# Optimization experiments

Hardware: AMD Instinct MI355X
Metric: run time of the kernel (lower is better)

Reference implementation:

```python
import jax, jax.numpy as jnp
import numpy as np

B = 1
FRAMES = 16
P = 64            # patch_dim = image_size // patch_size = 256 // 4
C = 512           # query_dim == hidden_dim
T, HW, WW = 2, 8, 8   # window_size
NH = 8            # num_heads
HD = C // NH      # head_dim = 64
N = FRAMES * P * P


def setup_inputs() -> dict:
    key = jax.random.key(0)
    ks = jax.random.split(key, 5)
    x = jax.random.normal(ks[0], (B, N, C), dtype=jnp.float32)
    Wq = jax.random.normal(ks[1], (C, C), dtype=jnp.float32) * 0.02
    Wk = jax.random.normal(ks[2], (C, C), dtype=jnp.float32) * 0.02
    Wv = jax.random.normal(ks[3], (C, C), dtype=jnp.float32) * 0.02
    Wo = jax.random.normal(ks[4], (C, C), dtype=jnp.float32) * 0.02
    bo = jnp.zeros((C,), dtype=jnp.float32)
    return {"x": x, "Wq": Wq, "Wk": Wk, "Wv": Wv, "Wo": Wo, "bo": bo}


def reference(x, Wq, Wk, Wv, Wo, bo):
    nT, nH, nW = FRAMES // T, P // HW, P // WW
    L = T * HW * WW            # tokens per window = 128
    NWIN = nT * nH * nW        # 512 windows

    # window partition: [B,N,C] -> [B,nWin,L,C]
    xw = x.reshape(B, nT, T, nH, HW, nW, WW, C)
    xw = xw.transpose(0, 1, 3, 5, 2, 4, 6, 7).reshape(B, NWIN, L, C)

    # QKV projections (torch Linear: y = x @ W.T), split heads
    q = (xw @ Wq.T).reshape(B, NWIN, L, NH, HD)
    k = (xw @ Wk.T).reshape(B, NWIN, L, NH, HD)
    v = (xw @ Wv.T).reshape(B, NWIN, L, NH, HD)

    scale = 1.0 / jnp.sqrt(jnp.float32(HD))
    attn = jnp.einsum('bwqhd,bwkhd->bwhqk', q, k) * scale
    attn = jax.nn.softmax(attn, axis=-1)
    out = jnp.einsum('bwhqk,bwkhd->bwqhd', attn, v).reshape(B, NWIN, L, C)

    out = out @ Wo.T + bo      # output projection (dropout is identity at p=0/eval)

    # window merge: inverse of partition
    y = out.reshape(B, nT, nH, nW, T, HW, WW, C)
    y = y.transpose(0, 1, 4, 2, 5, 3, 6, 7).reshape(B, N, C)
    return y
```

## Files before the change

### kernel.cpp

```cpp
#include <hip/hip_runtime.h>


typedef __bf16 bf16x8 __attribute__((ext_vector_type(8)));
typedef float  f32x4  __attribute__((ext_vector_type(4)));

__device__ __forceinline__ unsigned short f2bf(float f) {
    unsigned int u = __float_as_uint(f);
    u += 0x7FFFu + ((u >> 16) & 1u);
    return (unsigned short)(u >> 16);
}
__device__ __forceinline__ unsigned int pack2(float lo, float hi) {
    return (unsigned int)f2bf(lo) | ((unsigned int)f2bf(hi) << 16);
}
__device__ __forceinline__ void glds16(const void* g, void* l) {
    __builtin_amdgcn_global_load_lds(
        (const __attribute__((address_space(1))) unsigned int*)g,
        (__attribute__((address_space(3))) unsigned int*)l, 16, 0, 0);
}

__global__ __launch_bounds__(256) void gather_cvt(const float* __restrict__ x,
                                                  unsigned short* __restrict__ xbf) {
    int tid = blockIdx.x * 256 + threadIdx.x;
    int r = tid >> 6;
    int c = (tid & 63) << 3;
    int w = r >> 7, l = r & 127;
    int wt = w >> 6, wy = (w >> 3) & 7, wx = w & 7;
    int lt = l >> 6, ly = (l >> 3) & 7, lx = l & 7;
    size_t n = (size_t)(wt * 2 + lt) * 4096 + (size_t)(wy * 8 + ly) * 64 + (wx * 8 + lx);
    const float4* s = (const float4*)(x + n * 512 + c);
    float4 a = s[0], b = s[1];
    uint4 o;
    o.x = pack2(a.x, a.y); o.y = pack2(a.z, a.w);
    o.z = pack2(b.x, b.y); o.w = pack2(b.z, b.w);
    *(uint4*)(xbf + (size_t)r * 512 + c) = o;
}

__global__ __launch_bounds__(256) void cvt_w4(const float* __restrict__ Wq,
                                              const float* __restrict__ Wk,
                                              const float* __restrict__ Wv,
                                              const float* __restrict__ Wo,
                                              unsigned short* __restrict__ d) {
    int b = blockIdx.x >> 7;
    int tid = (blockIdx.x & 127) * 256 + threadIdx.x;
    const float* s = (b == 0) ? Wq : (b == 1) ? Wk : (b == 2) ? Wv : Wo;
    const float4* sp = (const float4*)s + (size_t)tid * 2;
    float4 a = sp[0], bb = sp[1];
    uint4 o;
    o.x = pack2(a.x, a.y); o.y = pack2(a.z, a.w);
    o.z = pack2(bb.x, bb.y); o.w = pack2(bb.z, bb.w);
    ((uint4*)(d + (size_t)b * 262144))[tid] = o;
}


#define STAGE_A(tt, kh) do {                                                   \
    const unsigned short* g_ = Ap + (size_t)(tt) * 64 + (kh) * 32 + gOff;      \
    unsigned short* l_ = smem + ((((tt) & 1) * 2 + (kh)) * 8192);              \
    glds16(g_, l_ + j * 8);                                                    \
    glds16(g_ + 65536, l_ + 4096 + j * 8);                                     \
  } while (0)

#define STAGE_B(tt, kh) do {                                                   \
    const unsigned short* g_ = Bp + (size_t)(tt) * 64 + (kh) * 32 + gOff;      \
    unsigned short* l_ = smem + 32768 + ((((tt) & 1) * 2 + (kh)) * 8192);      \
    glds16(g_, l_ + j * 8);                                                    \
    glds16(g_ + 65536, l_ + 4096 + j * 8);                                     \
  } while (0)

#define PH_READA(d, ks, mh)                                                    \
    _Pragma("unroll") for (int i_ = 0; i_ < 4; ++i_)                           \
      af[i_] = *(const bf16x8*)(smem + ((d) * 2 + (ks)) * 8192 +               \
                                (arow + (mh) * 64 + i_ * 16) * 32 + ech);

#define PH_READB(d, ks)                                                        \
    _Pragma("unroll") for (int n_ = 0; n_ < 4; ++n_)                           \
      bfr[n_] = *(const bf16x8*)(smem + 32768 + ((d) * 2 + (ks)) * 8192 +      \
                                 (brow + n_ * 16) * 32 + ech);

#define PH_MFMA(mh)                                                            \
    __builtin_amdgcn_s_barrier();                                              \
    asm volatile("s_waitcnt lgkmcnt(0)" ::: "memory");                         \
    __builtin_amdgcn_sched_barrier(0);                                         \
    __builtin_amdgcn_s_setprio(1);                                             \
    _Pragma("unroll") for (int n_ = 0; n_ < 4; ++n_)                           \
      _Pragma("unroll") for (int i_ = 0; i_ < 4; ++i_)                         \
        acc[(mh) * 4 + i_][n_] = __builtin_amdgcn_mfma_f32_16x16x32_bf16(      \
            af[i_], bfr[n_], acc[(mh) * 4 + i_][n_], 0, 0, 0);                 \
    __builtin_amdgcn_s_setprio(0);                                             \
    __builtin_amdgcn_s_barrier();

__global__ __launch_bounds__(512, 2) void qkv_gemm8(const unsigned short* __restrict__ xbf,
                                                    const unsigned short* __restrict__ wb,
                                                    unsigned short* __restrict__ Qb,
                                                    unsigned short* __restrict__ Kb,
                                                    unsigned short* __restrict__ Vb) {
    extern __shared__ unsigned short smem[];
    int id = blockIdx.x;
    int xcd = id & 7, rest = id >> 3;
    int rowblk = xcd * 32 + rest / 6;
    int colblk = rest % 6;

    const unsigned short* Ap = xbf + (size_t)rowblk * 131072;
    const unsigned short* Bp = wb + (size_t)colblk * 131072;

    int j = threadIdx.x;
    int lane = j & 63, wv = j >> 6;
    int wm = wv >> 2, wn = wv & 3;
    int quad = lane >> 4, lc = lane & 15;

    int r0 = j >> 2;
    int dcol = (((j & 3) ^ ((j >> 3) & 3)) << 3);
    const size_t gOff = (size_t)r0 * 512 + dcol;

    int arow = wm * 128 + lc;
    int brow = wn * 64 + lc;
    int ech = (quad ^ ((lc >> 1) & 3)) << 3;

    f32x4 acc[8][4] = {};
    bf16x8 af[4], bfr[4];

    STAGE_A(0, 0); STAGE_B(0, 0); STAGE_A(0, 1); STAGE_B(0, 1);
    STAGE_A(1, 0); STAGE_B(1, 0);
    asm volatile("s_waitcnt vmcnt(4)" ::: "memory");
    __builtin_amdgcn_s_barrier();

    #pragma unroll 2
    for (int t = 0; t < 8; ++t) {
        const int d = t & 1;
        PH_READA(d, 0, 0); PH_READB(d, 0);
        if (t < 7) STAGE_A(t + 1, 1);
        PH_MFMA(0);
        PH_READA(d, 0, 1);
        if (t < 7) {
            STAGE_B(t + 1, 1);
            asm volatile("s_waitcnt vmcnt(4)" ::: "memory");
        }
        PH_MFMA(1);
        PH_READA(d, 1, 0); PH_READB(d, 1);
        if (t < 6) STAGE_A(t + 2, 0);
        PH_MFMA(0);
        PH_READA(d, 1, 1);
        if (t < 6) {
            STAGE_B(t + 2, 0);
            asm volatile("s_waitcnt vmcnt(4)" ::: "memory");
        } else if (t == 6) {
            asm volatile("s_waitcnt vmcnt(0)" ::: "memory");
        }
        PH_MFMA(1);
    }

    unsigned short* sc = smem + wv * 8192;
    int cb = colblk * 256 + wn * 64;
    int pj = cb >> 9;
    int h = (cb >> 6) & 7;
    int w2 = rowblk * 2 + wm;
    size_t ob = ((size_t)w2 * 8 + h) * 8192;

    if (pj == 2) {
        #pragma unroll
        for (int mi = 0; mi < 8; ++mi)
            #pragma unroll
            for (int n = 0; n < 4; ++n)
                #pragma unroll
                for (int rg = 0; rg < 4; ++rg) {
                    int l = mi * 16 + quad * 4 + rg;
                    int d2 = n * 16 + lc;
                    sc[d2 * 128 + (((l >> 3) ^ (d2 & 7)) << 3) + (l & 7)] =
                        f2bf(acc[mi][n][rg]);
                }
        asm volatile("s_waitcnt lgkmcnt(0)" ::: "memory");
        #pragma unroll
        for (int i = 0; i < 16; ++i) {
            int ci = i * 64 + lane;
            int d2 = ci >> 4, k = ci & 15;
            uint4 val = *(const uint4*)(sc + d2 * 128 + ((k ^ (d2 & 7)) << 3));
            *(uint4*)(Vb + ob + (size_t)ci * 8) = val;
        }
    } else {
        unsigned short* outp = pj ? Kb : Qb;
        float s = pj ? 1.0f : 0.125f;
        #pragma unroll
        for (int mi = 0; mi < 8; ++mi)
            #pragma unroll
            for (int n = 0; n < 4; ++n)
                #pragma unroll
                for (int rg = 0; rg < 4; ++rg) {
                    int l = mi * 16 + quad * 4 + rg;
                    int d2 = n * 16 + lc;
                    sc[l * 64 + (((d2 >> 3) ^ (l & 7)) << 3) + (d2 & 7)] =
                        f2bf(acc[mi][n][rg] * s);
                }
        asm volatile("s_waitcnt lgkmcnt(0)" ::: "memory");
        #pragma unroll
        for (int i = 0; i < 16; ++i) {
            int ci = i * 64 + lane;
            int l = ci >> 3, k = ci & 7;
            uint4 val = *(const uint4*)(sc + l * 64 + ((k ^ (l & 7)) << 3));
            *(uint4*)(outp + ob + (size_t)ci * 8) = val;
        }
    }
}

__global__ __launch_bounds__(256) void attn(const unsigned short* __restrict__ Qb,
                                            const unsigned short* __restrict__ Kb,
                                            const unsigned short* __restrict__ Vb,
                                            unsigned short* __restrict__ O) {
    int h = blockIdx.x, w = blockIdx.y;
    size_t base = ((size_t)w * 8 + h) * 8192;
    const unsigned short* q = Qb + base;
    const unsigned short* k = Kb + base;
    const unsigned short* v = Vb + base;

    __shared__ unsigned short smem[24576];
    unsigned short* sV = smem;
    unsigned short* sQ = smem + 8192;
    unsigned short* sK = smem + 16384;
    unsigned short* sP = smem + 8192;

    int t = threadIdx.x, lane = t & 63, wv = t >> 6;
    int quad = lane >> 4, lc = lane & 15;
    int sw = lc & 7;

    #pragma unroll
    for (int i = 0; i < 4; i++) {
        int s = t + i * 256;
        int r = s >> 3;
        int cq = ((s & 7) ^ (r & 7)) * 8;
        glds16(q + (size_t)r * 64 + cq, sQ + s * 8);
        glds16(k + (size_t)r * 64 + cq, sK + s * 8);
        int rv = s >> 4;
        int cv = (((s & 15) ^ (rv & 7))) * 8;
        glds16(v + (size_t)rv * 128 + cv, sV + s * 8);
    }
    __syncthreads();

    f32x4 acc[2][8] = {};
    #pragma unroll
    for (int ks = 0; ks < 2; ks++) {
        int ch = ((quad + ks * 4) ^ sw) * 8;
        bf16x8 af[2];
        #pragma unroll
        for (int mi = 0; mi < 2; mi++)
            af[mi] = *(const bf16x8*)(&sQ[(wv * 32 + mi * 16 + lc) * 64 + ch]);
        #pragma unroll
        for (int ni = 0; ni < 8; ni++) {
            bf16x8 bfr = *(const bf16x8*)(&sK[(ni * 16 + lc) * 64 + ch]);
            #pragma unroll
            for (int mi = 0; mi < 2; mi++)
                acc[mi][ni] = __builtin_amdgcn_mfma_f32_16x16x32_bf16(af[mi], bfr, acc[mi][ni], 0, 0, 0);
        }
    }

    #pragma unroll
    for (int mi = 0; mi < 2; mi++)
        #pragma unroll
        for (int rg = 0; rg < 4; rg++) {
            float m = -1e30f;
            #pragma unroll
            for (int ni = 0; ni < 8; ni++) m = fmaxf(m, acc[mi][ni][rg]);
            #pragma unroll
            for (int off = 1; off < 16; off <<= 1) m = fmaxf(m, __shfl_xor(m, off, 64));
            float s = 0.f;
            #pragma unroll
            for (int ni = 0; ni < 8; ni++) {
                float e = __expf(acc[mi][ni][rg] - m);
                acc[mi][ni][rg] = e;
                s += e;
            }
            #pragma unroll
            for (int off = 1; off < 16; off <<= 1) s += __shfl_xor(s, off, 64);
            float inv = 1.0f / s;
            #pragma unroll
            for (int ni = 0; ni < 8; ni++) acc[mi][ni][rg] *= inv;
        }

    __syncthreads();
    #pragma unroll
    for (int mi = 0; mi < 2; mi++)
        #pragma unroll
        for (int ni = 0; ni < 8; ni++)
            #pragma unroll
            for (int rg = 0; rg < 4; rg++) {
                int r = wv * 32 + mi * 16 + quad * 4 + rg;
                int c = ni * 16 + lc;
                sP[r * 128 + (((c >> 3) ^ (r & 7)) << 3) + (c & 7)] = f2bf(acc[mi][ni][rg]);
            }
    __syncthreads();

    f32x4 oc[2][4] = {};
    #pragma unroll
    for (int ks = 0; ks < 4; ks++) {
        int ch = ((quad + ks * 4) ^ sw) * 8;
        bf16x8 af[2];
        #pragma unroll
        for (int mi = 0; mi < 2; mi++)
            af[mi] = *(const bf16x8*)(&sP[(wv * 32 + mi * 16 + lc) * 128 + ch]);
        #pragma unroll
        for (int ni = 0; ni < 4; ni++) {
            bf16x8 bfr = *(const bf16x8*)(&sV[(ni * 16 + lc) * 128 + ch]);
            #pragma unroll
            for (int mi = 0; mi < 2; mi++)
                oc[mi][ni] = __builtin_amdgcn_mfma_f32_16x16x32_bf16(af[mi], bfr, oc[mi][ni], 0, 0, 0);
        }
    }

    #pragma unroll
    for (int mi = 0; mi < 2; mi++)
        #pragma unroll
        for (int ni = 0; ni < 4; ni++)
            #pragma unroll
            for (int rg = 0; rg < 4; rg++) {
                int l = wv * 32 + mi * 16 + quad * 4 + rg;
                int d = ni * 16 + lc;
                O[((size_t)w * 128 + l) * 512 + h * 64 + d] = f2bf(oc[mi][ni][rg]);
            }
}

__global__ __launch_bounds__(256) void oproj_gemm(const unsigned short* __restrict__ A,
                                                  const unsigned short* __restrict__ Bw,
                                                  const float* __restrict__ bo,
                                                  float* __restrict__ out) {
    int id = blockIdx.x;
    int xcd = id & 7, rest = id >> 3;
    int rb = xcd * 64 + (rest >> 2);
    int nb = rest & 3;
    const unsigned short* Ab = A + (size_t)rb * 128 * 512;
    const unsigned short* Bb = Bw + (size_t)nb * 128 * 512;
    __shared__ unsigned short sA[128 * 64];
    __shared__ unsigned short sB[128 * 64];
    f32x4 acc[4][4] = {};
    int t = threadIdx.x, lane = t & 63, wv = t >> 6;
    int wm = wv & 1, wn = wv >> 1, quad = lane >> 4, lc = lane & 15;
    int sw = lc & 7;

    int sr = t >> 3;
    int gco = ((t & 7) ^ (sr & 7)) * 8;

    for (int k0 = 0; k0 < 512; k0 += 64) {
        __syncthreads();
        #pragma unroll
        for (int i = 0; i < 4; i++) {
            int r = sr + i * 32;
            glds16(Ab + (size_t)r * 512 + k0 + gco, sA + (t + i * 256) * 8);
            glds16(Bb + (size_t)r * 512 + k0 + gco, sB + (t + i * 256) * 8);
        }
        __syncthreads();
        #pragma unroll
        for (int ks = 0; ks < 2; ks++) {
            int ch = ((quad + ks * 4) ^ sw) * 8;
            bf16x8 af[4], bfr[4];
            #pragma unroll
            for (int i = 0; i < 4; i++) {
                af[i]  = *(const bf16x8*)(&sA[(wm * 64 + i * 16 + lc) * 64 + ch]);
                bfr[i] = *(const bf16x8*)(&sB[(wn * 64 + i * 16 + lc) * 64 + ch]);
            }
            #pragma unroll
            for (int mi = 0; mi < 4; mi++)
                #pragma unroll
                for (int ni = 0; ni < 4; ni++)
                    acc[mi][ni] = __builtin_amdgcn_mfma_f32_16x16x32_bf16(af[mi], bfr[ni], acc[mi][ni], 0, 0, 0);
        }
    }

    float bias[4];
    #pragma unroll
    for (int ni = 0; ni < 4; ni++)
        bias[ni] = bo[nb * 128 + wn * 64 + ni * 16 + lc];

    #pragma unroll
    for (int mi = 0; mi < 4; mi++)
        #pragma unroll
        for (int rg = 0; rg < 4; rg++) {
            int r = rb * 128 + wm * 64 + mi * 16 + quad * 4 + rg;
            int w = r >> 7, l = r & 127;
            int wt = w >> 6, wy = (w >> 3) & 7, wx = w & 7;
            int lt = l >> 6, ly = (l >> 3) & 7, lx = l & 7;
            size_t n = (size_t)(wt * 2 + lt) * 4096 + (size_t)(wy * 8 + ly) * 64 + (wx * 8 + lx);
            #pragma unroll
            for (int ni = 0; ni < 4; ni++) {
                int col = nb * 128 + wn * 64 + ni * 16 + lc;
                out[n * 512 + col] = acc[mi][ni][rg] + bias[ni];
            }
        }
}

extern "C" void kernel_launch(void* const* d_in, const int* in_sizes, int n_in,
                              void* d_out, int out_size, void* d_ws, size_t ws_size,
                              hipStream_t stream) {
    const float* x  = (const float*)d_in[0];
    const float* Wq = (const float*)d_in[1];
    const float* Wk = (const float*)d_in[2];
    const float* Wv = (const float*)d_in[3];
    const float* Wo = (const float*)d_in[4];
    const float* bo = (const float*)d_in[5];
    float* out = (float*)d_out;

    char* ws = (char*)d_ws;
    unsigned short* xbf = (unsigned short*)(ws);
    unsigned short* Qb  = (unsigned short*)(ws + 67108864);
    unsigned short* Kb  = (unsigned short*)(ws + 134217728);
    unsigned short* Vb  = (unsigned short*)(ws + 201326592);
    unsigned short* Wqb = (unsigned short*)(ws + 268435456);

    static bool attrset = false;
    if (!attrset) {
        (void)hipFuncSetAttribute(reinterpret_cast<const void*>(qkv_gemm8),
                                  hipFuncAttributeMaxDynamicSharedMemorySize, 131072);
        attrset = true;
    }

    gather_cvt<<<16384, 256, 0, stream>>>(x, xbf);
    cvt_w4<<<512, 256, 0, stream>>>(Wq, Wk, Wv, Wo, Wqb);

    qkv_gemm8<<<1536, 512, 131072, stream>>>(xbf, Wqb, Qb, Kb, Vb);
    attn<<<dim3(8, 512), 256, 0, stream>>>(Qb, Kb, Vb, xbf);
    oproj_gemm<<<2048, 256, 0, stream>>>(xbf, Wqb + 786432, bo, out);
}
```

Before: 474.0 us.

## Reuse pipelined 256x256 GEMM for output projection and shrink attention LDS

The output projection GEMM is rewritten to use the same 512-thread, 256x256-tile, double-buffered main loop as the QKV GEMM, shared through a macro. The 128x128 tile kernel it replaces synchronized on every K step. The attention kernel now loads Q fragments straight from global into registers and reuses the K buffer for P, processing P in two halves. This cuts LDS from 48KB to 32KB to raise occupancy. The cost is more register pressure, and the oproj grid drops to 512 large blocks, which may under-fill the device.

```diff
diff --git a/kernel.cpp b/kernel.cpp
--- a/kernel.cpp
+++ b/kernel.cpp
@@ -88,6 +88,36 @@
     __builtin_amdgcn_s_setprio(0);                                             \
     __builtin_amdgcn_s_barrier();
 
+#define GEMM8_MAIN_LOOP                                                        \
+    STAGE_A(0, 0); STAGE_B(0, 0); STAGE_A(0, 1); STAGE_B(0, 1);                \
+    STAGE_A(1, 0); STAGE_B(1, 0);                                              \
+    asm volatile("s_waitcnt vmcnt(4)" ::: "memory");                           \
+    __builtin_amdgcn_s_barrier();                                              \
+    _Pragma("unroll 2")                                                        \
+    for (int t = 0; t < 8; ++t) {                                              \
+        const int d = t & 1;                                                   \
+        PH_READA(d, 0, 0); PH_READB(d, 0);                                     \
+        if (t < 7) STAGE_A(t + 1, 1);                                          \
+        PH_MFMA(0);                                                            \
+        PH_READA(d, 0, 1);                                                     \
+        if (t < 7) {                                                           \
+            STAGE_B(t + 1, 1);                                                 \
+            asm volatile("s_waitcnt vmcnt(4)" ::: "memory");                   \
+        }                                                                      \
+        PH_MFMA(1);                                                            \
+        PH_READA(d, 1, 0); PH_READB(d, 1);                                     \
+        if (t < 6) STAGE_A(t + 2, 0);                                          \
+        PH_MFMA(0);                                                            \
+        PH_READA(d, 1, 1);                                                     \
+        if (t < 6) {                                                           \
+            STAGE_B(t + 2, 0);                                                 \
+            asm volatile("s_waitcnt vmcnt(4)" ::: "memory");                   \
+        } else if (t == 6) {                                                   \
+            asm volatile("s_waitcnt vmcnt(0)" ::: "memory");                   \
+        }                                                                      \
+        PH_MFMA(1);                                                            \
+    }
+
 __global__ __launch_bounds__(512, 2) void qkv_gemm8(const unsigned short* __restrict__ xbf,
                                                     const unsigned short* __restrict__ wb,
                                                     unsigned short* __restrict__ Qb,
@@ -118,35 +148,7 @@
     f32x4 acc[8][4] = {};
     bf16x8 af[4], bfr[4];
 
-    STAGE_A(0, 0); STAGE_B(0, 0); STAGE_A(0, 1); STAGE_B(0, 1);
-    STAGE_A(1, 0); STAGE_B(1, 0);
-    asm volatile("s_waitcnt vmcnt(4)" ::: "memory");
-    __builtin_amdgcn_s_barrier();
-
-    #pragma unroll 2
-    for (int t = 0; t < 8; ++t) {
-        const int d = t & 1;
-        PH_READA(d, 0, 0); PH_READB(d, 0);
-        if (t < 7) STAGE_A(t + 1, 1);
-        PH_MFMA(0);
-        PH_READA(d, 0, 1);
-        if (t < 7) {
-            STAGE_B(t + 1, 1);
-            asm volatile("s_waitcnt vmcnt(4)" ::: "memory");
-        }
-        PH_MFMA(1);
-        PH_READA(d, 1, 0); PH_READB(d, 1);
-        if (t < 6) STAGE_A(t + 2, 0);
-        PH_MFMA(0);
-        PH_READA(d, 1, 1);
-        if (t < 6) {
-            STAGE_B(t + 2, 0);
-            asm volatile("s_waitcnt vmcnt(4)" ::: "memory");
-        } else if (t == 6) {
-            asm volatile("s_waitcnt vmcnt(0)" ::: "memory");
-        }
-        PH_MFMA(1);
-    }
+    GEMM8_MAIN_LOOP
 
     unsigned short* sc = smem + wv * 8192;
     int cb = colblk * 256 + wn * 64;
@@ -210,11 +212,9 @@
     const unsigned short* k = Kb + base;
     const unsigned short* v = Vb + base;
 
-    __shared__ unsigned short smem[24576];
+    __shared__ unsigned short smem[16384];
     unsigned short* sV = smem;
-    unsigned short* sQ = smem + 8192;
-    unsigned short* sK = smem + 16384;
-    unsigned short* sP = smem + 8192;
+    unsigned short* sKP = smem + 8192;
 
     int t = threadIdx.x, lane = t & 63, wv = t >> 6;
     int quad = lane >> 4, lc = lane & 15;
@@ -225,28 +225,31 @@
         int s = t + i * 256;
         int r = s >> 3;
         int cq = ((s & 7) ^ (r & 7)) * 8;
-        glds16(q + (size_t)r * 64 + cq, sQ + s * 8);
-        glds16(k + (size_t)r * 64 + cq, sK + s * 8);
+        glds16(k + (size_t)r * 64 + cq, sKP + s * 8);
         int rv = s >> 4;
         int cv = (((s & 15) ^ (rv & 7))) * 8;
         glds16(v + (size_t)rv * 128 + cv, sV + s * 8);
     }
+
+    bf16x8 aq[2][2];
+    #pragma unroll
+    for (int mi = 0; mi < 2; mi++)
+        #pragma unroll
+        for (int ks = 0; ks < 2; ks++)
+            aq[mi][ks] = *(const bf16x8*)(q + (size_t)(wv * 32 + mi * 16 + lc) * 64 +
+                                          ks * 32 + quad * 8);
     __syncthreads();
 
     f32x4 acc[2][8] = {};
     #pragma unroll
     for (int ks = 0; ks < 2; ks++) {
         int ch = ((quad + ks * 4) ^ sw) * 8;
-        bf16x8 af[2];
-        #pragma unroll
-        for (int mi = 0; mi < 2; mi++)
-            af[mi] = *(const bf16x8*)(&sQ[(wv * 32 + mi * 16 + lc) * 64 + ch]);
         #pragma unroll
         for (int ni = 0; ni < 8; ni++) {
-            bf16x8 bfr = *(const bf16x8*)(&sK[(ni * 16 + lc) * 64 + ch]);
+            bf16x8 bfr = *(const bf16x8*)(&sKP[(ni * 16 + lc) * 64 + ch]);
             #pragma unroll
             for (int mi = 0; mi < 2; mi++)
-                acc[mi][ni] = __builtin_amdgcn_mfma_f32_16x16x32_bf16(af[mi], bfr, acc[mi][ni], 0, 0, 0);
+                acc[mi][ni] = __builtin_amdgcn_mfma_f32_16x16x32_bf16(aq[mi][ks], bfr, acc[mi][ni], 0, 0, 0);
         }
     }
 
@@ -274,32 +277,39 @@
         }
 
     __syncthreads();
-    #pragma unroll
-    for (int mi = 0; mi < 2; mi++)
-        #pragma unroll
-        for (int ni = 0; ni < 8; ni++)
-            #pragma unroll
-            for (int rg = 0; rg < 4; rg++) {
-                int r = wv * 32 + mi * 16 + quad * 4 + rg;
-                int c = ni * 16 + lc;
-                sP[r * 128 + (((c >> 3) ^ (r & 7)) << 3) + (c & 7)] = f2bf(acc[mi][ni][rg]);
+
+    f32x4 oc[2][4] = {};
+    #pragma unroll
+    for (int half = 0; half < 2; half++) {
+        #pragma unroll
+        for (int mi = 0; mi < 2; mi++)
+            #pragma unroll
+            for (int ni2 = 0; ni2 < 4; ni2++) {
+                int ni = half * 4 + ni2;
+                #pragma unroll
+                for (int rg = 0; rg < 4; rg++) {
+                    int r = wv * 32 + mi * 16 + quad * 4 + rg;
+                    int c = ni2 * 16 + lc;
+                    sKP[r * 64 + (((c >> 3) ^ (r & 7)) << 3) + (c & 7)] = f2bf(acc[mi][ni][rg]);
+                }
             }
-    __syncthreads();
-
-    f32x4 oc[2][4] = {};
-    #pragma unroll
-    for (int ks = 0; ks < 4; ks++) {
-        int ch = ((quad + ks * 4) ^ sw) * 8;
-        bf16x8 af[2];
-        #pragma unroll
-        for (int mi = 0; mi < 2; mi++)
-            af[mi] = *(const bf16x8*)(&sP[(wv * 32 + mi * 16 + lc) * 128 + ch]);
-        #pragma unroll
-        for (int ni = 0; ni < 4; ni++) {
-            bf16x8 bfr = *(const bf16x8*)(&sV[(ni * 16 + lc) * 128 + ch]);
+        asm volatile("s_waitcnt lgkmcnt(0)" ::: "memory");
+        __builtin_amdgcn_sched_barrier(0);
+        #pragma unroll
+        for (int ks2 = 0; ks2 < 2; ks2++) {
+            int chp = ((quad + ks2 * 4) ^ sw) * 8;
+            int chv = (half * 8 + ((ks2 * 4 + quad) ^ sw)) * 8;
+            bf16x8 af[2];
             #pragma unroll
             for (int mi = 0; mi < 2; mi++)
-                oc[mi][ni] = __builtin_amdgcn_mfma_f32_16x16x32_bf16(af[mi], bfr, oc[mi][ni], 0, 0, 0);
+                af[mi] = *(const bf16x8*)(&sKP[(wv * 32 + mi * 16 + lc) * 64 + chp]);
+            #pragma unroll
+            for (int ni = 0; ni < 4; ni++) {
+                bf16x8 bfr = *(const bf16x8*)(&sV[(ni * 16 + lc) * 128 + chv]);
+                #pragma unroll
+                for (int mi = 0; mi < 2; mi++)
+                    oc[mi][ni] = __builtin_amdgcn_mfma_f32_16x16x32_bf16(af[mi], bfr, oc[mi][ni], 0, 0, 0);
+            }
         }
     }
 
@@ -315,71 +325,55 @@
             }
 }
 
-__global__ __launch_bounds__(256) void oproj_gemm(const unsigned short* __restrict__ A,
-                                                  const unsigned short* __restrict__ Bw,
-                                                  const float* __restrict__ bo,
-                                                  float* __restrict__ out) {
+__global__ __launch_bounds__(512, 2) void oproj_gemm8(const unsigned short* __restrict__ A,
+                                                      const unsigned short* __restrict__ Bw,
+                                                      const float* __restrict__ bo,
+                                                      float* __restrict__ out) {
+    extern __shared__ unsigned short smem[];
     int id = blockIdx.x;
     int xcd = id & 7, rest = id >> 3;
-    int rb = xcd * 64 + (rest >> 2);
-    int nb = rest & 3;
-    const unsigned short* Ab = A + (size_t)rb * 128 * 512;
-    const unsigned short* Bb = Bw + (size_t)nb * 128 * 512;
-    __shared__ unsigned short sA[128 * 64];
-    __shared__ unsigned short sB[128 * 64];
-    f32x4 acc[4][4] = {};
-    int t = threadIdx.x, lane = t & 63, wv = t >> 6;
-    int wm = wv & 1, wn = wv >> 1, quad = lane >> 4, lc = lane & 15;
-    int sw = lc & 7;
-
-    int sr = t >> 3;
-    int gco = ((t & 7) ^ (sr & 7)) * 8;
-
-    for (int k0 = 0; k0 < 512; k0 += 64) {
-        __syncthreads();
-        #pragma unroll
-        for (int i = 0; i < 4; i++) {
-            int r = sr + i * 32;
-            glds16(Ab + (size_t)r * 512 + k0 + gco, sA + (t + i * 256) * 8);
-            glds16(Bb + (size_t)r * 512 + k0 + gco, sB + (t + i * 256) * 8);
-        }
-        __syncthreads();
-        #pragma unroll
-        for (int ks = 0; ks < 2; ks++) {
-            int ch = ((quad + ks * 4) ^ sw) * 8;
-            bf16x8 af[4], bfr[4];
-            #pragma unroll
-            for (int i = 0; i < 4; i++) {
-                af[i]  = *(const bf16x8*)(&sA[(wm * 64 + i * 16 + lc) * 64 + ch]);
-                bfr[i] = *(const bf16x8*)(&sB[(wn * 64 + i * 16 + lc) * 64 + ch]);
-            }
-            #pragma unroll
-            for (int mi = 0; mi < 4; mi++)
-                #pragma unroll
-                for (int ni = 0; ni < 4; ni++)
-                    acc[mi][ni] = __builtin_amdgcn_mfma_f32_16x16x32_bf16(af[mi], bfr[ni], acc[mi][ni], 0, 0, 0);
-        }
-    }
-
+    int rowblk = xcd * 32 + (rest >> 1);
+    int colblk = rest & 1;
+
+    const unsigned short* Ap = A + (size_t)rowblk * 131072;
+    const unsigned short* Bp = Bw + (size_t)colblk * 131072;
+
+    int j = threadIdx.x;
+    int lane = j & 63, wv = j >> 6;
+    int wm = wv >> 2, wn = wv & 3;
+    int quad = lane >> 4, lc = lane & 15;
+
+    int r0 = j >> 2;
+    int dcol = (((j & 3) ^ ((j >> 3) & 3)) << 3);
+    const size_t gOff = (size_t)r0 * 512 + dcol;
+
+    int arow = wm * 128 + lc;
+    int brow = wn * 64 + lc;
+    int ech = (quad ^ ((lc >> 1) & 3)) << 3;
+
+    f32x4 acc[8][4] = {};
+    bf16x8 af[4], bfr[4];
+
+    GEMM8_MAIN_LOOP
+
+    int cbase = colblk * 256 + wn * 64;
     float bias[4];
     #pragma unroll
     for (int ni = 0; ni < 4; ni++)
-        bias[ni] = bo[nb * 128 + wn * 64 + ni * 16 + lc];
-
-    #pragma unroll
-    for (int mi = 0; mi < 4; mi++)
-        #pragma unroll
-        for (int rg = 0; rg < 4; rg++) {
-            int r = rb * 128 + wm * 64 + mi * 16 + quad * 4 + rg;
+        bias[ni] = bo[cbase + ni * 16 + lc];
+
+    #pragma unroll
+    for (int mi = 0; mi < 8; ++mi)
+        #pragma unroll
+        for (int rg = 0; rg < 4; ++rg) {
+            int r = rowblk * 256 + wm * 128 + mi * 16 + quad * 4 + rg;
             int w = r >> 7, l = r & 127;
             int wt = w >> 6, wy = (w >> 3) & 7, wx = w & 7;
             int lt = l >> 6, ly = (l >> 3) & 7, lx = l & 7;
             size_t n = (size_t)(wt * 2 + lt) * 4096 + (size_t)(wy * 8 + ly) * 64 + (wx * 8 + lx);
             #pragma unroll
-            for (int ni = 0; ni < 4; ni++) {
-                int col = nb * 128 + wn * 64 + ni * 16 + lc;
-                out[n * 512 + col] = acc[mi][ni][rg] + bias[ni];
-            }
+            for (int ni = 0; ni < 4; ni++)
+                out[n * 512 + cbase + ni * 16 + lc] = acc[mi][ni][rg] + bias[ni];
         }
 }
 
@@ -405,6 +399,8 @@
     if (!attrset) {
         (void)hipFuncSetAttribute(reinterpret_cast<const void*>(qkv_gemm8),
                                   hipFuncAttributeMaxDynamicSharedMemorySize, 131072);
+        (void)hipFuncSetAttribute(reinterpret_cast<const void*>(oproj_gemm8),
+                                  hipFuncAttributeMaxDynamicSharedMemorySize, 131072);
         attrset = true;
     }
 
@@ -413,5 +409,5 @@
 
     qkv_gemm8<<<1536, 512, 131072, stream>>>(xbf, Wqb, Qb, Kb, Vb);
     attn<<<dim3(8, 512), 256, 0, stream>>>(Qb, Kb, Vb, xbf);
-    oproj_gemm<<<2048, 256, 0, stream>>>(xbf, Wqb + 786432, bo, out);
-}
+    oproj_gemm8<<<512, 512, 131072, stream>>>(xbf, Wqb + 786432, bo, out);
+}
```

New measurement: 474.4 us. No clear change (+0.1%).
